# Performance work log

Measured on AMD Instinct MI355X. Metric: run time of the kernel, lower is better.

Reference implementation:

```python
import jax, jax.numpy as jnp
import numpy as np
from jax import lax

VOCAB, EMB, HID, NCLS = 30000, 256, 256, 10


def setup_inputs() -> dict:
    key = jax.random.key(0)
    ks = jax.random.split(key, 12)
    B, T = 128, 512
    s_e = 1.0 / np.sqrt(EMB)
    s_h = 1.0 / np.sqrt(HID)
    inp = {
        "inputs": jax.random.randint(ks[0], (B, T), 0, VOCAB),
        "emb_table": jax.random.normal(ks[1], (VOCAB, EMB), jnp.float32),
        # forward-direction GRU params (torch layout: gates ordered r,z,n)
        "W_ih_f": jax.random.uniform(ks[2], (3 * HID, EMB), jnp.float32, -s_h, s_h),
        "W_hh_f": jax.random.uniform(ks[3], (3 * HID, HID), jnp.float32, -s_h, s_h),
        "b_ih_f": jax.random.uniform(ks[4], (3 * HID,), jnp.float32, -s_h, s_h),
        "b_hh_f": jax.random.uniform(ks[5], (3 * HID,), jnp.float32, -s_h, s_h),
        # backward-direction GRU params
        "W_ih_b": jax.random.uniform(ks[6], (3 * HID, EMB), jnp.float32, -s_h, s_h),
        "W_hh_b": jax.random.uniform(ks[7], (3 * HID, HID), jnp.float32, -s_h, s_h),
        "b_ih_b": jax.random.uniform(ks[8], (3 * HID,), jnp.float32, -s_h, s_h),
        "b_hh_b": jax.random.uniform(ks[9], (3 * HID,), jnp.float32, -s_h, s_h),
        # classifier head
        "W_lin": jax.random.uniform(ks[10], (NCLS, 2 * HID), jnp.float32, -1.0 / np.sqrt(2 * HID), 1.0 / np.sqrt(2 * HID)),
        "b_lin": jax.random.uniform(ks[11], (NCLS,), jnp.float32, -1.0 / np.sqrt(2 * HID), 1.0 / np.sqrt(2 * HID)),
    }
    return inp


def _gru_dir(x_tbe, W_ih, W_hh, b_ih, b_hh):
    """Run GRU over time-major x [T,B,E]; returns final hidden [B,H]."""
    # Precompute input projections for all steps in one big GEMM.
    xg = jnp.einsum("tbe,ge->tbg", x_tbe, W_ih) + b_ih  # [T,B,3H]

    def step(h, xg_t):
        hg = h @ W_hh.T + b_hh  # [B,3H]
        xr, xz, xn = jnp.split(xg_t, 3, axis=-1)
        hr, hz, hn = jnp.split(hg, 3, axis=-1)
        r = jax.nn.sigmoid(xr + hr)
        z = jax.nn.sigmoid(xz + hz)
        n = jnp.tanh(xn + r * hn)
        h_new = (1.0 - z) * n + z * h
        return h_new, None

    h0 = jnp.zeros((x_tbe.shape[1], W_hh.shape[1]), x_tbe.dtype)
    h_last, _ = lax.scan(step, h0, xg)
    return h_last


def reference(inputs, emb_table, W_ih_f, W_hh_f, b_ih_f, b_hh_f,
              W_ih_b, W_hh_b, b_ih_b, b_hh_b, W_lin, b_lin):
    # Dropout is identity in eval mode.
    emb = emb_table[inputs]               # [B,T,E]
    x = jnp.transpose(emb, (1, 0, 2))     # time-major [T,B,E]
    h_f = _gru_dir(x, W_ih_f, W_hh_f, b_ih_f, b_hh_f)            # [B,H]
    h_b = _gru_dir(x[::-1], W_ih_b, W_hh_b, b_ih_b, b_hh_b)      # [B,H]
    hidden = jnp.concatenate([h_f, h_b], axis=-1)                 # [B,2H]
    return hidden @ W_lin.T + b_lin                               # [B,10]
```

## Files before the change

kernel.cpp:

```cpp
#include <hip/hip_runtime.h>


typedef float f32x4 __attribute__((ext_vector_type(4)));
typedef short s16x8 __attribute__((ext_vector_type(8)));

#define VOCAB   30000
#define GCOLS   1536
#define HB_STR  280
#define HBUF    (16 * HB_STR)
#define GP_STR  1032
#define HS_STR  260
#define SRF     (-1.4426950408889634f)
#define SNF     (2.8853900817779268f)

#if defined(__has_builtin)
#if __has_builtin(__builtin_amdgcn_cvt_pk_bf16_f32)
#define HAVE_PK 1
#endif
#endif

static __device__ __forceinline__ unsigned short f2bf(float f) {
    unsigned u = __builtin_bit_cast(unsigned, f);
    u += 0x7fffu + ((u >> 16) & 1u);
    return (unsigned short)(u >> 16);
}
#ifdef HAVE_PK
typedef __bf16 bf16x2_t __attribute__((ext_vector_type(2)));
static __device__ __forceinline__ unsigned pk2(float a, float b) {
    bf16x2_t v = __builtin_amdgcn_cvt_pk_bf16_f32(a, b);
    return __builtin_bit_cast(unsigned, v);
}
#else
static __device__ __forceinline__ unsigned pk2(float a, float b) {
    return (unsigned)f2bf(a) | ((unsigned)f2bf(b) << 16);
}
#endif
static __device__ __forceinline__ float bf_lo(unsigned v) {
    return __builtin_bit_cast(float, v << 16);
}
static __device__ __forceinline__ float bf_hi(unsigned v) {
    return __builtin_bit_cast(float, v & 0xffff0000u);
}
static __device__ __forceinline__ s16x8 pack_bf8(float4 a, float4 b, float s) {
    union { s16x8 v; unsigned u[4]; } r;
    r.u[0] = pk2(a.x * s, a.y * s); r.u[1] = pk2(a.z * s, a.w * s);
    r.u[2] = pk2(b.x * s, b.y * s); r.u[3] = pk2(b.z * s, b.w * s);
    return r.v;
}
static __device__ __forceinline__ f32x4 mfma16(s16x8 a, s16x8 b, f32x4 c) {
    return __builtin_amdgcn_mfma_f32_16x16x32_bf16(a, b, c, 0, 0, 0);
}
static __device__ __forceinline__ float sig2(float x) {
    return __builtin_amdgcn_rcpf(1.0f + __builtin_amdgcn_exp2f(x));
}
static __device__ __forceinline__ void gload_lds16(const unsigned short* g, unsigned short* l) {
    __builtin_amdgcn_global_load_lds(
        (const __attribute__((address_space(1))) unsigned*)g,
        (__attribute__((address_space(3))) unsigned*)l, 16, 0, 0);
}


__global__ __launch_bounds__(512, 2)
void gru_table_kernel(const float* __restrict__ emb,
                      const float* __restrict__ Wih_f, const float* __restrict__ bih_f,
                      const float* __restrict__ bhh_f,
                      const float* __restrict__ Wih_b, const float* __restrict__ bih_b,
                      const float* __restrict__ bhh_b,
                      unsigned short* __restrict__ G) {
    __shared__ unsigned short aS[2][16 * HB_STR];

    const int tid  = threadIdx.x;
    const int lane = tid & 63;
    const int w    = tid >> 6;
    const int u    = lane & 15;
    const int q    = lane >> 4;
    const int d    = blockIdx.x;
    const int by   = blockIdx.y;

    const float* Wih = d ? Wih_b : Wih_f;
    const float* bih = d ? bih_b : bih_f;
    const float* bhh = d ? bhh_b : bhh_f;

    s16x8 breg[48];
    float beta[6];
#pragma unroll
    for (int t = 0; t < 6; ++t) {
        const int orig = (t >> 1) * 256 + 32 * w + ((t & 1) << 4) + u;
        const float scl = (t < 4) ? SRF : SNF;
        beta[t] = (bih[orig] + ((t < 4) ? bhh[orig] : 0.0f)) * scl;
#pragma unroll
        for (int kt = 0; kt < 8; ++kt) {
            const float* p = Wih + orig * 256 + kt * 32 + q * 8;
            breg[t * 8 + kt] =
                pack_bf8(*(const float4*)p, *(const float4*)(p + 4), scl);
        }
    }

    const int srow = tid >> 5;
    const int sc8  = (tid & 31) * 8;

    {
        const float* p = emb + (size_t)(by * 16 + srow) * 256 + sc8;
        float4 e0 = *(const float4*)p, e1 = *(const float4*)(p + 4);
        unsigned* dp = (unsigned*)&aS[0][srow * HB_STR + sc8];
        dp[0] = pk2(e0.x, e0.y); dp[1] = pk2(e0.z, e0.w);
        dp[2] = pk2(e1.x, e1.y); dp[3] = pk2(e1.z, e1.w);
    }
    __syncthreads();

    const size_t colbase = (size_t)(d * 48 + 6 * w) * 16 + u;

    for (int i = 0;; ++i) {
        const int mt = by + i * 128;
        if (mt >= 1875) break;
        const int mtn = mt + 128;
        const bool has_next = (mtn < 1875);
        const int buf = i & 1;

        float4 e0, e1;
        if (has_next) {
            const float* p = emb + (size_t)(mtn * 16 + srow) * 256 + sc8;
            e0 = *(const float4*)p;
            e1 = *(const float4*)(p + 4);
        }

        const int v0 = mt * 16;
#pragma unroll
        for (int l = 0; l < 2; ++l) {
            f32x4 a0 = {0.f, 0.f, 0.f, 0.f}, a1 = a0, a2 = a0;
#pragma unroll
            for (int kt = 0; kt < 8; ++kt) {
                s16x8 af = *(const s16x8*)&aS[buf][u * HB_STR + kt * 32 + q * 8];
                a0 = mfma16(af, breg[(0 + l) * 8 + kt], a0);
                a1 = mfma16(af, breg[(2 + l) * 8 + kt], a1);
                a2 = mfma16(af, breg[(4 + l) * 8 + kt], a2);
            }
#pragma unroll
            for (int g = 0; g < 3; ++g) {
                const f32x4 a = (g == 0) ? a0 : (g == 1) ? a1 : a2;
                const int t = 2 * g + l;
                unsigned short* gp = G + (size_t)(v0 + q * 4) * GCOLS + colbase + t * 16;
#pragma unroll
                for (int r = 0; r < 4; ++r)
                    gp[(size_t)r * GCOLS] = f2bf(a[r] + beta[t]);
            }
        }
        if (has_next) {
            unsigned* dp = (unsigned*)&aS[buf ^ 1][srow * HB_STR + sc8];
            dp[0] = pk2(e0.x, e0.y); dp[1] = pk2(e0.z, e0.w);
            dp[2] = pk2(e1.x, e1.y); dp[3] = pk2(e1.z, e1.w);
        }
        __syncthreads();
    }
}

__global__ __launch_bounds__(512, 2)
void gru_rnn_kernel(const int* __restrict__ inp,
                    const float* __restrict__ Whh_f, const float* __restrict__ bhh_f,
                    const float* __restrict__ Whh_b, const float* __restrict__ bhh_b,
                    const float* __restrict__ W_lin, const float* __restrict__ b_lin,
                    const unsigned short* __restrict__ G,
                    float* __restrict__ out) {
    __shared__ int            toks[16][513];
    __shared__ unsigned short hB[2 * HBUF];
    __shared__ unsigned short xgS[2][16][GP_STR];
    __shared__ float          bhnS[256];
    __shared__ float          hs[16 * HS_STR];

    const int tid  = threadIdx.x;
    const int lane = tid & 63;
    const int w    = tid >> 6;
    const int b    = lane & 15;
    const int q    = lane >> 4;
    const int d    = blockIdx.x >> 3;
    const int b0   = (blockIdx.x & 7) * 16;

    const float* Whh = d ? Whh_b : Whh_f;
    const float* bhh = d ? bhh_b : bhh_f;

    s16x8 wreg[48];
#pragma unroll
    for (int t = 0; t < 6; ++t) {
        const int orig = (t >> 1) * 256 + 32 * w + ((t & 1) << 4) + b;
        const float scl = (t < 4) ? SRF : SNF;
#pragma unroll
        for (int kt = 0; kt < 8; ++kt) {
            const float* p = Whh + orig * 256 + kt * 32 + q * 8;
            wreg[t * 8 + kt] =
                pack_bf8(*(const float4*)p, *(const float4*)(p + 4), scl);
        }
    }

    for (int i = tid; i < 16 * 512; i += 512) {
        int bb = i >> 9, t = i & 511;
        toks[bb][t] = inp[(b0 + bb) * 512 + t];
    }
    for (int i = tid; i < 2 * HBUF; i += 512) hB[i] = 0;
    if (tid < 256) bhnS[tid] = SNF * bhh[512 + tid];
    __syncthreads();

    {
        int t0 = d ? 511 : 0;
#pragma unroll
        for (int j = 0; j < 2; ++j) {
            int bb = 2 * w + j;
            int tok = toks[bb][t0];
            const unsigned short* gb = G + (size_t)tok * GCOLS + (d ? 512 : 0) + lane * 8;
            gload_lds16(gb,       &xgS[0][bb][0]);
            gload_lds16(gb + 512, &xgS[0][bb][512]);
        }
    }
    __syncthreads();

    const int xoff = d ? 256 : 0;
    const int hbq  = b * HB_STR + q * 8;
    float hreg[8];
#pragma unroll
    for (int i = 0; i < 8; ++i) hreg[i] = 0.f;

#pragma unroll 2
    for (int ts = 0; ts < 512; ++ts) {
        const int rb = (ts & 1) * HBUF;
        const int pn = (ts + 1) & 1;
        {
            int s1 = (ts < 511) ? ts + 1 : 511;
            int t1 = d ? 511 - s1 : s1;
#pragma unroll
            for (int j = 0; j < 2; ++j) {
                int bb = 2 * w + j;
                int tok = toks[bb][t1];
                const unsigned short* gb = G + (size_t)tok * GCOLS + (d ? 512 : 0) + lane * 8;
                gload_lds16(gb,       &xgS[pn][bb][0]);
                gload_lds16(gb + 512, &xgS[pn][bb][512]);
            }
        }
        const unsigned short* xrow = &xgS[ts & 1][b][xoff + 96 * w + 4 * q];
        uint2 uxr0 = *(const uint2*)&xrow[0];
        uint2 uxz0 = *(const uint2*)&xrow[32];
        uint2 uxn0 = *(const uint2*)&xrow[64];
        uint2 uxr1 = *(const uint2*)&xrow[16];
        uint2 uxz1 = *(const uint2*)&xrow[48];
        uint2 uxn1 = *(const uint2*)&xrow[80];

#pragma unroll
        for (int l = 0; l < 2; ++l) {
            const uint2 uxr = l ? uxr1 : uxr0;
            const uint2 uxz = l ? uxz1 : uxz0;
            const uint2 uxn = l ? uxn1 : uxn0;
            float xr[4] = {bf_lo(uxr.x), bf_hi(uxr.x), bf_lo(uxr.y), bf_hi(uxr.y)};
            float xz[4] = {bf_lo(uxz.x), bf_hi(uxz.x), bf_lo(uxz.y), bf_hi(uxz.y)};
            float xn[4] = {bf_lo(uxn.x), bf_hi(uxn.x), bf_lo(uxn.y), bf_hi(uxn.y)};

            f32x4 ar = {0.f, 0.f, 0.f, 0.f};
            f32x4 az = {0.f, 0.f, 0.f, 0.f};
#pragma unroll
            for (int kt = 0; kt < 8; ++kt) {
                s16x8 hf = *(const s16x8*)&hB[rb + hbq + kt * 32];
                ar = mfma16(wreg[(0 + l) * 8 + kt], hf, ar);
                az = mfma16(wreg[(2 + l) * 8 + kt], hf, az);
            }
            f32x4 an = *(const f32x4*)&bhnS[32 * w + 16 * l + 4 * q];
#pragma unroll
            for (int kt = 0; kt < 8; ++kt) {
                s16x8 hf = *(const s16x8*)&hB[rb + hbq + kt * 32];
                an = mfma16(wreg[(4 + l) * 8 + kt], hf, an);
            }
            float rg[4], zg[4];
#pragma unroll
            for (int r = 0; r < 4; ++r) {
                rg[r] = sig2(xr[r] + ar[r]);
                zg[r] = sig2(xz[r] + az[r]);
            }
#pragma unroll
            for (int r = 0; r < 4; ++r) {
                float tg = sig2(fmaf(rg[r], an[r], xn[r]));
                float ng = fmaf(-2.0f, tg, 1.0f);
                const int i = l * 4 + r;
                hreg[i] = fmaf(zg[r], hreg[i] - ng, ng);
            }
            unsigned p0 = pk2(hreg[l * 4 + 0], hreg[l * 4 + 1]);
            unsigned p1 = pk2(hreg[l * 4 + 2], hreg[l * 4 + 3]);
            *(uint2*)&hB[pn * HBUF + b * HB_STR + 32 * w + 16 * l + 4 * q] =
                make_uint2(p0, p1);
        }
        __syncthreads();
    }

#pragma unroll
    for (int l = 0; l < 2; ++l) {
        f32x4 v = {hreg[l * 4 + 0], hreg[l * 4 + 1],
                   hreg[l * 4 + 2], hreg[l * 4 + 3]};
        *(f32x4*)&hs[b * HS_STR + 32 * w + 16 * l + 4 * q] = v;
    }
    __syncthreads();
    if (tid < 160) {
        int bb = tid / 10;
        int c  = tid - bb * 10;
        float acc = d ? 0.0f : b_lin[c];
        const float* wl = W_lin + c * 512 + d * 256;
        const float* hp = &hs[bb * HS_STR];
        for (int i = 0; i < 256; ++i) acc += hp[i] * wl[i];
        atomicAdd(&out[(b0 + bb) * 10 + c], acc);
    }
}

extern "C" void kernel_launch(void* const* d_in, const int* in_sizes, int n_in,
                              void* d_out, int out_size, void* d_ws, size_t ws_size,
                              hipStream_t stream) {
    const int*   inp   = (const int*)d_in[0];
    const float* emb   = (const float*)d_in[1];
    const float* Wih_f = (const float*)d_in[2];
    const float* Whh_f = (const float*)d_in[3];
    const float* bih_f = (const float*)d_in[4];
    const float* bhh_f = (const float*)d_in[5];
    const float* Wih_b = (const float*)d_in[6];
    const float* Whh_b = (const float*)d_in[7];
    const float* bih_b = (const float*)d_in[8];
    const float* bhh_b = (const float*)d_in[9];
    const float* W_lin = (const float*)d_in[10];
    const float* b_lin = (const float*)d_in[11];
    float* out = (float*)d_out;
    unsigned short* G = (unsigned short*)d_ws;

    hipMemsetAsync(d_out, 0, (size_t)out_size * sizeof(float), stream);
    hipLaunchKernelGGL(gru_table_kernel, dim3(2, 128), dim3(512), 0, stream,
                       emb, Wih_f, bih_f, bhh_f, Wih_b, bih_b, bhh_b, G);
    hipLaunchKernelGGL(gru_rnn_kernel, dim3(16), dim3(512), 0, stream,
                       inp, Whh_f, bhh_f, Whh_b, bhh_b, W_lin, b_lin, G, out);
}
```

Before: 1.065 ms.

## Reorder gate table per lane and prefetch input gates into registers

```diff
diff --git a/kernel.cpp b/kernel.cpp
--- a/kernel.cpp
+++ b/kernel.cpp
@@ -8,7 +8,6 @@
 #define GCOLS   1536
 #define HB_STR  280
 #define HBUF    (16 * HB_STR)
-#define GP_STR  1032
 #define HS_STR  260
 #define SRF     (-1.4426950408889634f)
 #define SNF     (2.8853900817779268f)
@@ -53,12 +52,13 @@
 static __device__ __forceinline__ float sig2(float x) {
     return __builtin_amdgcn_rcpf(1.0f + __builtin_amdgcn_exp2f(x));
 }
-static __device__ __forceinline__ void gload_lds16(const unsigned short* g, unsigned short* l) {
-    __builtin_amdgcn_global_load_lds(
-        (const __attribute__((address_space(1))) unsigned*)g,
-        (__attribute__((address_space(3))) unsigned*)l, 16, 0, 0);
-}
-
+static __device__ __forceinline__ void lgkm_barrier() {
+    __builtin_amdgcn_sched_barrier(0);
+    asm volatile("s_waitcnt lgkmcnt(0)" ::: "memory");
+    __builtin_amdgcn_sched_barrier(0);
+    __builtin_amdgcn_s_barrier();
+    __builtin_amdgcn_sched_barrier(0);
+}
 
 __global__ __launch_bounds__(512, 2)
 void gru_table_kernel(const float* __restrict__ emb,
@@ -108,7 +108,7 @@
     }
     __syncthreads();
 
-    const size_t colbase = (size_t)(d * 48 + 6 * w) * 16 + u;
+    const int ubase = ((d * 8 + w) * 4 + (u >> 2)) * 24 + (u & 3);
 
     for (int i = 0;; ++i) {
         const int mt = by + i * 128;
@@ -138,8 +138,10 @@
 #pragma unroll
             for (int g = 0; g < 3; ++g) {
                 const f32x4 a = (g == 0) ? a0 : (g == 1) ? a1 : a2;
-                const int t = 2 * g + l;
-                unsigned short* gp = G + (size_t)(v0 + q * 4) * GCOLS + colbase + t * 16;
+                const int t    = 2 * g + l;
+                const int slot = (g < 2) ? (8 * l + 4 * g) : (16 + 4 * l);
+                unsigned short* gp =
+                    G + (size_t)(v0 + q * 4) * GCOLS + ubase + slot;
 #pragma unroll
                 for (int r = 0; r < 4; ++r)
                     gp[(size_t)r * GCOLS] = f2bf(a[r] + beta[t]);
@@ -163,7 +165,6 @@
                     float* __restrict__ out) {
     __shared__ int            toks[16][513];
     __shared__ unsigned short hB[2 * HBUF];
-    __shared__ unsigned short xgS[2][16][GP_STR];
     __shared__ float          bhnS[256];
     __shared__ float          hs[16 * HS_STR];
 
@@ -199,60 +200,47 @@
     if (tid < 256) bhnS[tid] = SNF * bhh[512 + tid];
     __syncthreads();
 
+    const int hbq = b * HB_STR + q * 8;
+    const unsigned short* Gt = G + (size_t)(((d * 8 + w) * 4 + q) * 24);
+
+    float hreg[8];
+#pragma unroll
+    for (int i = 0; i < 8; ++i) hreg[i] = 0.f;
+
+    uint4 p0, p1, pnx;
     {
-        int t0 = d ? 511 : 0;
-#pragma unroll
-        for (int j = 0; j < 2; ++j) {
-            int bb = 2 * w + j;
-            int tok = toks[bb][t0];
-            const unsigned short* gb = G + (size_t)tok * GCOLS + (d ? 512 : 0) + lane * 8;
-            gload_lds16(gb,       &xgS[0][bb][0]);
-            gload_lds16(gb + 512, &xgS[0][bb][512]);
-        }
-    }
-    __syncthreads();
-
-    const int xoff = d ? 256 : 0;
-    const int hbq  = b * HB_STR + q * 8;
-    float hreg[8];
-#pragma unroll
-    for (int i = 0; i < 8; ++i) hreg[i] = 0.f;
+        const int tt = d ? 511 : 0;
+        const unsigned short* gb = Gt + (size_t)toks[b][tt] * GCOLS;
+        p0  = *(const uint4*)(gb);
+        p1  = *(const uint4*)(gb + 8);
+        pnx = *(const uint4*)(gb + 16);
+    }
 
 #pragma unroll 2
     for (int ts = 0; ts < 512; ++ts) {
         const int rb = (ts & 1) * HBUF;
-        const int pn = (ts + 1) & 1;
+        const int wb = ((ts + 1) & 1) * HBUF;
+
+        f32x4 arI0 = {bf_lo(p0.x), bf_hi(p0.x), bf_lo(p0.y), bf_hi(p0.y)};
+        f32x4 azI0 = {bf_lo(p0.z), bf_hi(p0.z), bf_lo(p0.w), bf_hi(p0.w)};
+        f32x4 arI1 = {bf_lo(p1.x), bf_hi(p1.x), bf_lo(p1.y), bf_hi(p1.y)};
+        f32x4 azI1 = {bf_lo(p1.z), bf_hi(p1.z), bf_lo(p1.w), bf_hi(p1.w)};
+        const uint4 nn = pnx;
+
         {
-            int s1 = (ts < 511) ? ts + 1 : 511;
-            int t1 = d ? 511 - s1 : s1;
-#pragma unroll
-            for (int j = 0; j < 2; ++j) {
-                int bb = 2 * w + j;
-                int tok = toks[bb][t1];
-                const unsigned short* gb = G + (size_t)tok * GCOLS + (d ? 512 : 0) + lane * 8;
-                gload_lds16(gb,       &xgS[pn][bb][0]);
-                gload_lds16(gb + 512, &xgS[pn][bb][512]);
-            }
-        }
-        const unsigned short* xrow = &xgS[ts & 1][b][xoff + 96 * w + 4 * q];
-        uint2 uxr0 = *(const uint2*)&xrow[0];
-        uint2 uxz0 = *(const uint2*)&xrow[32];
-        uint2 uxn0 = *(const uint2*)&xrow[64];
-        uint2 uxr1 = *(const uint2*)&xrow[16];
-        uint2 uxz1 = *(const uint2*)&xrow[48];
-        uint2 uxn1 = *(const uint2*)&xrow[80];
+            const int s1 = (ts < 511) ? ts + 1 : 511;
+            const int tt = d ? 511 - s1 : s1;
+            const unsigned short* gb = Gt + (size_t)toks[b][tt] * GCOLS;
+            p0  = *(const uint4*)(gb);
+            p1  = *(const uint4*)(gb + 8);
+            pnx = *(const uint4*)(gb + 16);
+        }
 
 #pragma unroll
         for (int l = 0; l < 2; ++l) {
-            const uint2 uxr = l ? uxr1 : uxr0;
-            const uint2 uxz = l ? uxz1 : uxz0;
-            const uint2 uxn = l ? uxn1 : uxn0;
-            float xr[4] = {bf_lo(uxr.x), bf_hi(uxr.x), bf_lo(uxr.y), bf_hi(uxr.y)};
-            float xz[4] = {bf_lo(uxz.x), bf_hi(uxz.x), bf_lo(uxz.y), bf_hi(uxz.y)};
-            float xn[4] = {bf_lo(uxn.x), bf_hi(uxn.x), bf_lo(uxn.y), bf_hi(uxn.y)};
-
-            f32x4 ar = {0.f, 0.f, 0.f, 0.f};
-            f32x4 az = {0.f, 0.f, 0.f, 0.f};
+            f32x4 ar = l ? arI1 : arI0;
+            f32x4 az = l ? azI1 : azI0;
+            __builtin_amdgcn_s_setprio(1);
 #pragma unroll
             for (int kt = 0; kt < 8; ++kt) {
                 s16x8 hf = *(const s16x8*)&hB[rb + hbq + kt * 32];
@@ -265,12 +253,17 @@
                 s16x8 hf = *(const s16x8*)&hB[rb + hbq + kt * 32];
                 an = mfma16(wreg[(4 + l) * 8 + kt], hf, an);
             }
+            __builtin_amdgcn_s_setprio(0);
+
             float rg[4], zg[4];
 #pragma unroll
             for (int r = 0; r < 4; ++r) {
-                rg[r] = sig2(xr[r] + ar[r]);
-                zg[r] = sig2(xz[r] + az[r]);
-            }
+                rg[r] = sig2(ar[r]);
+                zg[r] = sig2(az[r]);
+            }
+            const unsigned nx0 = l ? nn.z : nn.x;
+            const unsigned nx1 = l ? nn.w : nn.y;
+            const float xn[4] = {bf_lo(nx0), bf_hi(nx0), bf_lo(nx1), bf_hi(nx1)};
 #pragma unroll
             for (int r = 0; r < 4; ++r) {
                 float tg = sig2(fmaf(rg[r], an[r], xn[r]));
@@ -278,12 +271,12 @@
                 const int i = l * 4 + r;
                 hreg[i] = fmaf(zg[r], hreg[i] - ng, ng);
             }
-            unsigned p0 = pk2(hreg[l * 4 + 0], hreg[l * 4 + 1]);
-            unsigned p1 = pk2(hreg[l * 4 + 2], hreg[l * 4 + 3]);
-            *(uint2*)&hB[pn * HBUF + b * HB_STR + 32 * w + 16 * l + 4 * q] =
-                make_uint2(p0, p1);
-        }
-        __syncthreads();
+            unsigned h0 = pk2(hreg[l * 4 + 0], hreg[l * 4 + 1]);
+            unsigned h1 = pk2(hreg[l * 4 + 2], hreg[l * 4 + 3]);
+            *(uint2*)&hB[wb + b * HB_STR + 32 * w + 16 * l + 4 * q] =
+                make_uint2(h0, h1);
+        }
+        lgkm_barrier();
     }
 
 #pragma unroll
```

Result: slower. 1.562 ms (+46.7%).
